# Kernel optimization log

Measured on AMD Instinct MI355X. Metric: run time of the kernel, lower is better.

Reference implementation:

```python
import jax, jax.numpy as jnp
import numpy as np

LN_EPS = 1e-5

def setup_inputs() -> dict:
    key = jax.random.key(0)
    k1, k2, k3 = jax.random.split(key, 3)
    B, Lq, Lk, D = 16, 2048, 2048, 128
    return {
        "query": jax.random.normal(k1, (B, Lq, D), dtype=jnp.float32),
        "key": jax.random.normal(k2, (B, Lk, D), dtype=jnp.float32),
        "value": jax.random.normal(k3, (B, Lk, D), dtype=jnp.float32),
        "attn_mask": jnp.zeros((Lq, Lk), dtype=jnp.float32),
        "gamma": jnp.ones((D,), dtype=jnp.float32),
        "beta": jnp.zeros((D,), dtype=jnp.float32),
    }

def reference(query, key, value, attn_mask, gamma, beta):
    # NOTE: original code does NOT scale by 1/sqrt(d) despite the class name.
    scores = jnp.einsum("bqd,bkd->bqk", query, key)          # [B,Lq,Lk]
    scores = scores + attn_mask[None, :, :]
    probs = jax.nn.softmax(scores, axis=-1)
    out = jnp.einsum("bqk,bkd->bqd", probs, value)            # [B,Lq,D]
    # dropout is identity (eval / rate 0)
    mu = jnp.mean(out, axis=-1, keepdims=True)
    var = jnp.var(out, axis=-1, keepdims=True)
    normed = (out - mu) * jax.lax.rsqrt(var + LN_EPS)
    return normed * gamma + beta
```

## Files before the change

kernel.cpp:

```cpp
#include <hip/hip_runtime.h>
#include <hip/hip_bf16.h>
#include <hip/hip_fp16.h>
#include <math.h>

#define LQ_  2048
#define LK_  2048
#define D_   128
#define B_   16
#define LN_EPS 1e-5f
#define TK_  32
#define NTILE (LK_ / TK_)

#define KH_TILE_US 4096
#define VT_TILE_U  2048
#define KH_BYTES   ((size_t)B_ * NTILE * KH_TILE_US * 2)
#define VT_OFF     KH_BYTES

typedef __attribute__((ext_vector_type(8))) short short8;
typedef __attribute__((ext_vector_type(8))) _Float16 half8;
typedef __attribute__((ext_vector_type(4))) float f32x4;

union FragU { uint4 u4; short8 s8; half8 h8; unsigned int u[4]; };

__device__ __forceinline__ unsigned int pk_bf16(float a, float b) {
  __hip_bfloat162 h = __float22bfloat162_rn(make_float2(a, b));
  unsigned int u;
  __builtin_memcpy(&u, &h, 4);
  return u;
}
__device__ __forceinline__ unsigned short bf16_bits(float x) {
  return (unsigned short)(pk_bf16(x, 0.f) & 0xffffu);
}
__device__ __forceinline__ unsigned int pk_f16(float a, float b) {
  __half2 h = __floats2half2_rn(a, b);
  unsigned int u;
  __builtin_memcpy(&u, &h, 4);
  return u;
}
__device__ __forceinline__ float f16_lo(unsigned int u) {
  unsigned short s = (unsigned short)(u & 0xffffu);
  __half h; __builtin_memcpy(&h, &s, 2); return __half2float(h);
}
__device__ __forceinline__ float f16_hi(unsigned int u) {
  unsigned short s = (unsigned short)(u >> 16);
  __half h; __builtin_memcpy(&h, &s, 2); return __half2float(h);
}

__device__ __forceinline__ int idxK(int row, int d) {
  return row * 128 + ((((d >> 3) ^ row) & 15) << 3) + (d & 7);
}
__device__ __forceinline__ int idxVt(int d, int kp) {
  return d * 16 + ((((kp >> 2) + (d >> 1)) & 3) << 2) + (kp & 3);
}
__device__ __forceinline__ int idxPs(int row, int col) {
  return row * 32 + ((((col >> 3) ^ (row >> 2)) & 3) << 3) + (col & 7);
}

__device__ __forceinline__ void barrier_stage() {
  asm volatile("s_waitcnt vmcnt(8) lgkmcnt(0)\n\ts_barrier" ::: "memory");
}
__device__ __forceinline__ void fence_lds_local() {
  asm volatile("s_waitcnt lgkmcnt(0)" ::: "memory");
}

__device__ __forceinline__ void gld_lds16(const void* g, void* l) {
  __builtin_amdgcn_global_load_lds((const __attribute__((address_space(1))) void*)g,
                                   (__attribute__((address_space(3))) void*)l, 16, 0, 0);
}

__global__ __launch_bounds__(256) void conv_kv(
    const float* __restrict__ kg, const float* __restrict__ vg,
    unsigned short* __restrict__ khg, unsigned int* __restrict__ vtg)
{
  __shared__ float Vlt[128 * 33];
  const int tid = threadIdx.x;
  const int blk = blockIdx.x;
  const int b = blk >> 6;
  const int t = blk & 63;

  const float* ks = kg + ((size_t)b * LK_ + t * 32) * D_;
  const float* vs = vg + ((size_t)b * LK_ + t * 32) * D_;
  unsigned short* kh = khg + (size_t)blk * KH_TILE_US;
  unsigned int*   vt = vtg + (size_t)blk * VT_TILE_U;

#pragma unroll
  for (int it = 0; it < 2; it++) {
    const int item = tid + it * 256;
    const int row = item >> 4;
    const int c8  = item & 15;
    const float* p = ks + row * D_ + c8 * 8;
    float4 x = *(const float4*)(p);
    float4 y = *(const float4*)(p + 4);
    FragU H;
    H.u[0] = pk_f16(x.x, x.y); H.u[1] = pk_f16(x.z, x.w);
    H.u[2] = pk_f16(y.x, y.y); H.u[3] = pk_f16(y.z, y.w);
    *(uint4*)&kh[idxK(row, c8 * 8)] = H.u4;
  }

#pragma unroll
  for (int i = 0; i < 4; i++) {
    const int item = tid + i * 256;
    const int r = item >> 5, c4 = item & 31;
    float4 x = *(const float4*)&vs[r * D_ + c4 * 4];
    Vlt[(c4 * 4 + 0) * 33 + r] = x.x;
    Vlt[(c4 * 4 + 1) * 33 + r] = x.y;
    Vlt[(c4 * 4 + 2) * 33 + r] = x.z;
    Vlt[(c4 * 4 + 3) * 33 + r] = x.w;
  }
  __syncthreads();

#pragma unroll
  for (int i = 0; i < 8; i++) {
    const int o = tid + i * 256;
    const int d = o >> 4, s = o & 15;
    const int gq = s >> 2, c = s & 3;
    const int kp = (((gq - (d >> 1)) & 3) << 2) | c;
    vt[o] = pk_bf16(Vlt[d * 33 + 2 * kp], Vlt[d * 33 + 2 * kp + 1]);
  }
}

__device__ __forceinline__ void stage_tile(int w, int lane,
    const unsigned short* khT, const unsigned int* vtT,
    int tile, unsigned short* khs, unsigned int* vts)
{
  const char* gkh = (const char*)(khT + (size_t)tile * KH_TILE_US);
  const char* gvt = (const char*)(vtT + (size_t)tile * VT_TILE_U);
#pragma unroll
  for (int c = 0; c < 2; c++) {
    const int off = (w + 4 * c) << 10;
    gld_lds16(gkh + off + lane * 16, (char*)khs + off);
    gld_lds16(gvt + off + lane * 16, (char*)vts + off);
  }
}

__global__ __launch_bounds__(256, 2) void attn_ln_mfma(
    const float* __restrict__ qg, const float* __restrict__ maskg,
    const float* __restrict__ gammag, const float* __restrict__ betag,
    const unsigned short* __restrict__ khg, const unsigned int* __restrict__ vtg,
    float* __restrict__ outg)
{
  __shared__ unsigned short KhS[2][32 * 128];
  __shared__ unsigned int   VtW[2][128 * 16];
  __shared__ unsigned short PsS[64 * 32];

  const int tid  = threadIdx.x;
  const int w    = tid >> 6;
  const int lane = tid & 63;
  const int quad = lane >> 4;
  const int lr   = lane & 15;

  const int id   = blockIdx.x;
  const int xcd  = id & 7;
  const int slot = id >> 3;
  const int b    = xcd * 2 + (slot >> 5);
  const int q0   = (slot & 31) * 64;

  const unsigned short* khT = khg + (size_t)b * NTILE * KH_TILE_US;
  const unsigned int*   vtT = vtg + (size_t)b * NTILE * VT_TILE_U;

  const float* mbase = maskg + (size_t)(q0 + w * 16 + quad * 4) * LK_ + lr;

  stage_tile(w, lane, khT, vtT, 0, &KhS[0][0], &VtW[0][0]);
  float mA[2][4], mB[2][4];
#pragma unroll
  for (int ct = 0; ct < 2; ct++)
#pragma unroll
    for (int reg = 0; reg < 4; reg++)
      mA[ct][reg] = mbase[(size_t)reg * LK_ + ct * 16];

  half8 qh[4], ql[4];
  {
    const float* qrow = qg + ((size_t)b * LQ_ + q0 + w * 16 + lr) * D_ + quad * 8;
#pragma unroll
    for (int c = 0; c < 4; c++) {
      float4 x = *(const float4*)(qrow + c * 32);
      float4 y = *(const float4*)(qrow + c * 32 + 4);
      FragU H, L;
      H.u[0] = pk_f16(x.x, x.y); H.u[1] = pk_f16(x.z, x.w);
      H.u[2] = pk_f16(y.x, y.y); H.u[3] = pk_f16(y.z, y.w);
      L.u[0] = pk_f16(x.x - f16_lo(H.u[0]), x.y - f16_hi(H.u[0]));
      L.u[1] = pk_f16(x.z - f16_lo(H.u[1]), x.w - f16_hi(H.u[1]));
      L.u[2] = pk_f16(y.x - f16_lo(H.u[2]), y.y - f16_hi(H.u[2]));
      L.u[3] = pk_f16(y.z - f16_lo(H.u[3]), y.w - f16_hi(H.u[3]));
      qh[c] = H.h8; ql[c] = L.h8;
    }
  }

  float l_part[4] = {0.f, 0.f, 0.f, 0.f};
  f32x4 o[8];
  const f32x4 zf = {0.f, 0.f, 0.f, 0.f};
#pragma unroll
  for (int n = 0; n < 8; n++) o[n] = zf;

  auto body = [&](int kt, int cur, float (&mu)[2][4], float (&mp)[2][4])
      __attribute__((always_inline)) -> void {
    const unsigned short* khc = &KhS[cur][0];
    const unsigned int*   vtc = &VtW[cur][0];

    barrier_stage();

    if (kt + 1 < NTILE) {
      stage_tile(w, lane, khT, vtT, kt + 1, &KhS[cur ^ 1][0], &VtW[cur ^ 1][0]);
#pragma unroll
      for (int ct = 0; ct < 2; ct++)
#pragma unroll
        for (int reg = 0; reg < 4; reg++)
          mp[ct][reg] = mbase[(size_t)reg * LK_ + (kt + 1) * TK_ + ct * 16];
    }

    f32x4 sH[2], sL[2];
    sH[0] = zf; sH[1] = zf; sL[0] = zf; sL[1] = zf;
#pragma unroll
    for (int c = 0; c < 4; c++) {
#pragma unroll
      for (int ct = 0; ct < 2; ct++) {
        FragU kh;
        kh.u4 = *(const uint4*)&khc[idxK(ct * 16 + lr, c * 32 + quad * 8)];
        sH[ct] = __builtin_amdgcn_mfma_f32_16x16x32_f16(qh[c], kh.h8, sH[ct], 0, 0, 0);
        sL[ct] = __builtin_amdgcn_mfma_f32_16x16x32_f16(ql[c], kh.h8, sL[ct], 0, 0, 0);
      }
    }

    FragU Bv[8];
#pragma unroll
    for (int nb = 0; nb < 8; nb++)
      Bv[nb].u4 = *(const uint4*)&vtc[idxVt(nb * 16 + lr, quad * 4)];

#pragma unroll
    for (int ct = 0; ct < 2; ct++)
#pragma unroll
      for (int reg = 0; reg < 4; reg++) {
        float s = sH[ct][reg] + sL[ct][reg];
        float p = __expf(s + mu[ct][reg]);
        l_part[reg] += p;
        PsS[idxPs(w * 16 + quad * 4 + reg, ct * 16 + lr)] = bf16_bits(p);
      }

    fence_lds_local();

    FragU A;
    A.u4 = *(const uint4*)&PsS[idxPs(w * 16 + lr, quad * 8)];
#pragma unroll
    for (int nb = 0; nb < 8; nb++)
      o[nb] = __builtin_amdgcn_mfma_f32_16x16x32_bf16(A.s8, Bv[nb].s8, o[nb], 0, 0, 0);
  };

  for (int kt = 0; kt < NTILE; kt += 2) {
    body(kt,     0, mA, mB);
    body(kt + 1, 1, mB, mA);
  }

  float inv_l[4];
#pragma unroll
  for (int reg = 0; reg < 4; reg++) {
    float l = l_part[reg];
#pragma unroll
    for (int m = 1; m <= 8; m <<= 1) l += __shfl_xor(l, m, 64);
    inv_l[reg] = 1.f / l;
  }

  float gam[8], bet[8];
#pragma unroll
  for (int nb = 0; nb < 8; nb++) {
    gam[nb] = gammag[nb * 16 + lr];
    bet[nb] = betag[nb * 16 + lr];
  }

#pragma unroll
  for (int reg = 0; reg < 4; reg++) {
    float s1 = 0.f, s2 = 0.f;
#pragma unroll
    for (int nb = 0; nb < 8; nb++) {
      float v = o[nb][reg] * inv_l[reg];
      o[nb][reg] = v;
      s1 += v; s2 += v * v;
    }
#pragma unroll
    for (int m = 1; m <= 8; m <<= 1) {
      s1 += __shfl_xor(s1, m, 64);
      s2 += __shfl_xor(s2, m, 64);
    }
    const float mean = s1 * (1.f / 128.f);
    const float var  = s2 * (1.f / 128.f) - mean * mean;
    const float rstd = rsqrtf(var + LN_EPS);

    float* op = outg + ((size_t)b * LQ_ + q0 + w * 16 + quad * 4 + reg) * D_ + lr;
#pragma unroll
    for (int nb = 0; nb < 8; nb++)
      op[nb * 16] = (o[nb][reg] - mean) * rstd * gam[nb] + bet[nb];
  }
}

extern "C" void kernel_launch(void* const* d_in, const int* in_sizes, int n_in,
                              void* d_out, int out_size, void* d_ws, size_t ws_size,
                              hipStream_t stream) {
  const float* q     = (const float*)d_in[0];
  const float* k     = (const float*)d_in[1];
  const float* v     = (const float*)d_in[2];
  const float* mask  = (const float*)d_in[3];
  const float* gamma = (const float*)d_in[4];
  const float* beta  = (const float*)d_in[5];
  float* out = (float*)d_out;

  unsigned short* khg = (unsigned short*)d_ws;
  unsigned int*   vtg = (unsigned int*)((char*)d_ws + VT_OFF);

  conv_kv<<<dim3(B_ * NTILE), dim3(256), 0, stream>>>(k, v, khg, vtg);
  attn_ln_mfma<<<dim3(512), dim3(256), 0, stream>>>(q, mask, gamma, beta,
                                                    khg, vtg, out);
}
```

Measured before the change: 174.4 us.

## Split key tiles across two wave groups per block with LDS reduction

Doubles the block to 512 threads and has two groups of four waves each process alternating key tiles for the same 64 query rows, with separate double-buffered LDS staging per group. After the loop, the second group writes its partial output accumulators and row sums to LDS and the first group adds them before normalization and LayerNorm. This aims to raise waves per CU and halve the serial key loop per block, at the cost of more LDS, an extra reduction phase and idle waves in the epilogue.

Result: slower. 414.4 us (+137.6%).

```diff
diff --git a/kernel.cpp b/kernel.cpp
--- a/kernel.cpp
+++ b/kernel.cpp
@@ -10,11 +10,14 @@
 #define LN_EPS 1e-5f
 #define TK_  32
 #define NTILE (LK_ / TK_)
+#define NBODY (NTILE / 2)
 
 #define KH_TILE_US 4096
 #define VT_TILE_U  2048
 #define KH_BYTES   ((size_t)B_ * NTILE * KH_TILE_US * 2)
 #define VT_OFF     KH_BYTES
+
+#define LDS_TOTAL 73728
 
 typedef __attribute__((ext_vector_type(8))) short short8;
 typedef __attribute__((ext_vector_type(8))) _Float16 half8;
@@ -58,6 +61,9 @@
 
 __device__ __forceinline__ void barrier_stage() {
   asm volatile("s_waitcnt vmcnt(8) lgkmcnt(0)\n\ts_barrier" ::: "memory");
+}
+__device__ __forceinline__ void barrier_lds() {
+  asm volatile("s_waitcnt lgkmcnt(0)\n\ts_barrier" ::: "memory");
 }
 __device__ __forceinline__ void fence_lds_local() {
   asm volatile("s_waitcnt lgkmcnt(0)" ::: "memory");
@@ -119,32 +125,32 @@
   }
 }
 
-__device__ __forceinline__ void stage_tile(int w, int lane,
+__device__ __forceinline__ void stage_tile(int wr, int lane,
     const unsigned short* khT, const unsigned int* vtT,
-    int tile, unsigned short* khs, unsigned int* vts)
+    int tile, char* khs, char* vts)
 {
   const char* gkh = (const char*)(khT + (size_t)tile * KH_TILE_US);
   const char* gvt = (const char*)(vtT + (size_t)tile * VT_TILE_U);
 #pragma unroll
   for (int c = 0; c < 2; c++) {
-    const int off = (w + 4 * c) << 10;
-    gld_lds16(gkh + off + lane * 16, (char*)khs + off);
-    gld_lds16(gvt + off + lane * 16, (char*)vts + off);
-  }
-}
-
-__global__ __launch_bounds__(256, 2) void attn_ln_mfma(
+    const int off = (wr + 4 * c) << 10;
+    gld_lds16(gkh + off + lane * 16, khs + off);
+    gld_lds16(gvt + off + lane * 16, vts + off);
+  }
+}
+
+__global__ __launch_bounds__(512, 4) void attn_ln_mfma(
     const float* __restrict__ qg, const float* __restrict__ maskg,
     const float* __restrict__ gammag, const float* __restrict__ betag,
     const unsigned short* __restrict__ khg, const unsigned int* __restrict__ vtg,
     float* __restrict__ outg)
 {
-  __shared__ unsigned short KhS[2][32 * 128];
-  __shared__ unsigned int   VtW[2][128 * 16];
-  __shared__ unsigned short PsS[64 * 32];
+  __shared__ __align__(16) char LB[LDS_TOTAL];
 
   const int tid  = threadIdx.x;
   const int w    = tid >> 6;
+  const int ts   = w >> 2;
+  const int wr   = w & 3;
   const int lane = tid & 63;
   const int quad = lane >> 4;
   const int lr   = lane & 15;
@@ -158,19 +164,25 @@
   const unsigned short* khT = khg + (size_t)b * NTILE * KH_TILE_US;
   const unsigned int*   vtT = vtg + (size_t)b * NTILE * VT_TILE_U;
 
-  const float* mbase = maskg + (size_t)(q0 + w * 16 + quad * 4) * LK_ + lr;
-
-  stage_tile(w, lane, khT, vtT, 0, &KhS[0][0], &VtW[0][0]);
+  char* khB0 = LB + (ts * 2 + 0) * 8192;
+  char* khB1 = LB + (ts * 2 + 1) * 8192;
+  char* vtB0 = LB + 32768 + (ts * 2 + 0) * 8192;
+  char* vtB1 = LB + 32768 + (ts * 2 + 1) * 8192;
+  unsigned short* Ps = (unsigned short*)(LB + 65536);
+
+  const float* mbase = maskg + (size_t)(q0 + wr * 16 + quad * 4) * LK_ + lr;
+
+  stage_tile(wr, lane, khT, vtT, ts, khB0, vtB0);
   float mA[2][4], mB[2][4];
 #pragma unroll
   for (int ct = 0; ct < 2; ct++)
 #pragma unroll
     for (int reg = 0; reg < 4; reg++)
-      mA[ct][reg] = mbase[(size_t)reg * LK_ + ct * 16];
+      mA[ct][reg] = mbase[(size_t)reg * LK_ + ts * TK_ + ct * 16];
 
   half8 qh[4], ql[4];
   {
-    const float* qrow = qg + ((size_t)b * LQ_ + q0 + w * 16 + lr) * D_ + quad * 8;
+    const float* qrow = qg + ((size_t)b * LQ_ + q0 + wr * 16 + lr) * D_ + quad * 8;
 #pragma unroll
     for (int c = 0; c < 4; c++) {
       float4 x = *(const float4*)(qrow + c * 32);
@@ -192,20 +204,21 @@
 #pragma unroll
   for (int n = 0; n < 8; n++) o[n] = zf;
 
-  auto body = [&](int kt, int cur, float (&mu)[2][4], float (&mp)[2][4])
+  auto body = [&](int i, int cur, float (&mu)[2][4], float (&mp)[2][4])
       __attribute__((always_inline)) -> void {
-    const unsigned short* khc = &KhS[cur][0];
-    const unsigned int*   vtc = &VtW[cur][0];
+    const unsigned short* khc = (const unsigned short*)(cur ? khB1 : khB0);
+    const unsigned int*   vtc = (const unsigned int*)(cur ? vtB1 : vtB0);
+    const int mt = 2 * i + ts;
 
     barrier_stage();
 
-    if (kt + 1 < NTILE) {
-      stage_tile(w, lane, khT, vtT, kt + 1, &KhS[cur ^ 1][0], &VtW[cur ^ 1][0]);
+    if (i + 1 < NBODY) {
+      stage_tile(wr, lane, khT, vtT, mt + 2, cur ? khB0 : khB1, cur ? vtB0 : vtB1);
 #pragma unroll
       for (int ct = 0; ct < 2; ct++)
 #pragma unroll
         for (int reg = 0; reg < 4; reg++)
-          mp[ct][reg] = mbase[(size_t)reg * LK_ + (kt + 1) * TK_ + ct * 16];
+          mp[ct][reg] = mbase[(size_t)reg * LK_ + (mt + 2) * TK_ + ct * 16];
     }
 
     f32x4 sH[2], sL[2];
@@ -233,61 +246,87 @@
         float s = sH[ct][reg] + sL[ct][reg];
         float p = __expf(s + mu[ct][reg]);
         l_part[reg] += p;
-        PsS[idxPs(w * 16 + quad * 4 + reg, ct * 16 + lr)] = bf16_bits(p);
+        Ps[idxPs(w * 16 + quad * 4 + reg, ct * 16 + lr)] = bf16_bits(p);
       }
 
     fence_lds_local();
 
     FragU A;
-    A.u4 = *(const uint4*)&PsS[idxPs(w * 16 + lr, quad * 8)];
+    A.u4 = *(const uint4*)&Ps[idxPs(w * 16 + lr, quad * 8)];
 #pragma unroll
     for (int nb = 0; nb < 8; nb++)
       o[nb] = __builtin_amdgcn_mfma_f32_16x16x32_bf16(A.s8, Bv[nb].s8, o[nb], 0, 0, 0);
   };
 
-  for (int kt = 0; kt < NTILE; kt += 2) {
-    body(kt,     0, mA, mB);
-    body(kt + 1, 1, mB, mA);
-  }
-
-  float inv_l[4];
-#pragma unroll
-  for (int reg = 0; reg < 4; reg++) {
-    float l = l_part[reg];
-#pragma unroll
-    for (int m = 1; m <= 8; m <<= 1) l += __shfl_xor(l, m, 64);
-    inv_l[reg] = 1.f / l;
-  }
-
-  float gam[8], bet[8];
-#pragma unroll
-  for (int nb = 0; nb < 8; nb++) {
-    gam[nb] = gammag[nb * 16 + lr];
-    bet[nb] = betag[nb * 16 + lr];
-  }
-
-#pragma unroll
-  for (int reg = 0; reg < 4; reg++) {
-    float s1 = 0.f, s2 = 0.f;
+  for (int i = 0; i < NBODY; i += 2) {
+    body(i,     0, mA, mB);
+    body(i + 1, 1, mB, mA);
+  }
+
+  float* exch = (float*)LB + (size_t)wr * 64 * 37 + (size_t)lane * 37;
+
+  barrier_lds();
+  if (ts == 1) {
+#pragma unroll
+    for (int nb = 0; nb < 8; nb++)
+#pragma unroll
+      for (int reg = 0; reg < 4; reg++)
+        exch[nb * 4 + reg] = o[nb][reg];
+#pragma unroll
+    for (int reg = 0; reg < 4; reg++)
+      exch[32 + reg] = l_part[reg];
+  }
+  barrier_lds();
+
+  if (ts == 0) {
+#pragma unroll
+    for (int nb = 0; nb < 8; nb++)
+#pragma unroll
+      for (int reg = 0; reg < 4; reg++)
+        o[nb][reg] += exch[nb * 4 + reg];
+#pragma unroll
+    for (int reg = 0; reg < 4; reg++)
+      l_part[reg] += exch[32 + reg];
+
+    float inv_l[4];
+#pragma unroll
+    for (int reg = 0; reg < 4; reg++) {
+      float l = l_part[reg];
+#pragma unroll
+      for (int m = 1; m <= 8; m <<= 1) l += __shfl_xor(l, m, 64);
+      inv_l[reg] = 1.f / l;
+    }
+
+    float gam[8], bet[8];
 #pragma unroll
     for (int nb = 0; nb < 8; nb++) {
-      float v = o[nb][reg] * inv_l[reg];
-      o[nb][reg] = v;
-      s1 += v; s2 += v * v;
-    }
-#pragma unroll
-    for (int m = 1; m <= 8; m <<= 1) {
-      s1 += __shfl_xor(s1, m, 64);
-      s2 += __shfl_xor(s2, m, 64);
-    }
-    const float mean = s1 * (1.f / 128.f);
-    const float var  = s2 * (1.f / 128.f) - mean * mean;
-    const float rstd = rsqrtf(var + LN_EPS);
-
-    float* op = outg + ((size_t)b * LQ_ + q0 + w * 16 + quad * 4 + reg) * D_ + lr;
-#pragma unroll
-    for (int nb = 0; nb < 8; nb++)
-      op[nb * 16] = (o[nb][reg] - mean) * rstd * gam[nb] + bet[nb];
+      gam[nb] = gammag[nb * 16 + lr];
+      bet[nb] = betag[nb * 16 + lr];
+    }
+
+#pragma unroll
+    for (int reg = 0; reg < 4; reg++) {
+      float s1 = 0.f, s2 = 0.f;
+#pragma unroll
+      for (int nb = 0; nb < 8; nb++) {
+        float v = o[nb][reg] * inv_l[reg];
+        o[nb][reg] = v;
+        s1 += v; s2 += v * v;
+      }
+#pragma unroll
+      for (int m = 1; m <= 8; m <<= 1) {
+        s1 += __shfl_xor(s1, m, 64);
+        s2 += __shfl_xor(s2, m, 64);
+      }
+      const float mean = s1 * (1.f / 128.f);
+      const float var  = s2 * (1.f / 128.f) - mean * mean;
+      const float rstd = rsqrtf(var + LN_EPS);
+
+      float* op = outg + ((size_t)b * LQ_ + q0 + wr * 16 + quad * 4 + reg) * D_ + lr;
+#pragma unroll
+      for (int nb = 0; nb < 8; nb++)
+        op[nb * 16] = (o[nb][reg] - mean) * rstd * gam[nb] + bet[nb];
+    }
   }
 }
 
@@ -306,6 +345,6 @@
   unsigned int*   vtg = (unsigned int*)((char*)d_ws + VT_OFF);
 
   conv_kv<<<dim3(B_ * NTILE), dim3(256), 0, stream>>>(k, v, khg, vtg);
-  attn_ln_mfma<<<dim3(512), dim3(256), 0, stream>>>(q, mask, gamma, beta,
+  attn_ln_mfma<<<dim3(512), dim3(512), 0, stream>>>(q, mask, gamma, beta,
                                                     khg, vtg, out);
 }
```

## Swap QK MFMA operands to keep P in registers and skip the LDS round-trip

Applied to the files above, without the earlier changes.

Computes S transposed by swapping the MFMA A and B operands, so each lane holds probabilities in the layout the PV MFMA needs as its A fragment. P is then packed into bf16 in registers, which removes the PsS shared buffer, its stores and reload, and the LDS fence. V^T is repacked in the prep kernel so its k ordering matches the new P fragment order. The mask is now loaded as float4 per row, and the row sum is reduced across quads and then redistributed with shuffles. The waitcnt threshold is also changed to vmcnt(2) to match the fewer outstanding loads.

New measurement: 182.0 us. 1.04x slower.

```diff
diff --git a/kernel.cpp b/kernel.cpp
--- a/kernel.cpp
+++ b/kernel.cpp
@@ -28,9 +28,6 @@
   __builtin_memcpy(&u, &h, 4);
   return u;
 }
-__device__ __forceinline__ unsigned short bf16_bits(float x) {
-  return (unsigned short)(pk_bf16(x, 0.f) & 0xffffu);
-}
 __device__ __forceinline__ unsigned int pk_f16(float a, float b) {
   __half2 h = __floats2half2_rn(a, b);
   unsigned int u;
@@ -49,18 +46,12 @@
 __device__ __forceinline__ int idxK(int row, int d) {
   return row * 128 + ((((d >> 3) ^ row) & 15) << 3) + (d & 7);
 }
-__device__ __forceinline__ int idxVt(int d, int kp) {
-  return d * 16 + ((((kp >> 2) + (d >> 1)) & 3) << 2) + (kp & 3);
-}
-__device__ __forceinline__ int idxPs(int row, int col) {
-  return row * 32 + ((((col >> 3) ^ (row >> 2)) & 3) << 3) + (col & 7);
+__device__ __forceinline__ int idxVt(int d, int slot) {
+  return d * 16 + ((((slot >> 2) + (d >> 1)) & 3) << 2) + (slot & 3);
 }
 
 __device__ __forceinline__ void barrier_stage() {
-  asm volatile("s_waitcnt vmcnt(8) lgkmcnt(0)\n\ts_barrier" ::: "memory");
-}
-__device__ __forceinline__ void fence_lds_local() {
-  asm volatile("s_waitcnt lgkmcnt(0)" ::: "memory");
+  asm volatile("s_waitcnt vmcnt(2) lgkmcnt(0)\n\ts_barrier" ::: "memory");
 }
 
 __device__ __forceinline__ void gld_lds16(const void* g, void* l) {
@@ -112,24 +103,25 @@
 #pragma unroll
   for (int i = 0; i < 8; i++) {
     const int o = tid + i * 256;
-    const int d = o >> 4, s = o & 15;
-    const int gq = s >> 2, c = s & 3;
-    const int kp = (((gq - (d >> 1)) & 3) << 2) | c;
+    const int d = o >> 4, sp = o & 15;
+    const int gl = ((sp >> 2) - (d >> 1)) & 3;
+    const int c  = sp & 3;
+    const int kp = 2 * gl + ((c >> 1) << 3) + (c & 1);
     vt[o] = pk_bf16(Vlt[d * 33 + 2 * kp], Vlt[d * 33 + 2 * kp + 1]);
   }
 }
 
 __device__ __forceinline__ void stage_tile(int w, int lane,
     const unsigned short* khT, const unsigned int* vtT,
-    int tile, unsigned short* khs, unsigned int* vts)
+    int tile, char* khs, char* vts)
 {
   const char* gkh = (const char*)(khT + (size_t)tile * KH_TILE_US);
   const char* gvt = (const char*)(vtT + (size_t)tile * VT_TILE_U);
 #pragma unroll
   for (int c = 0; c < 2; c++) {
     const int off = (w + 4 * c) << 10;
-    gld_lds16(gkh + off + lane * 16, (char*)khs + off);
-    gld_lds16(gvt + off + lane * 16, (char*)vts + off);
+    gld_lds16(gkh + off + lane * 16, khs + off);
+    gld_lds16(gvt + off + lane * 16, vts + off);
   }
 }
 
@@ -141,7 +133,6 @@
 {
   __shared__ unsigned short KhS[2][32 * 128];
   __shared__ unsigned int   VtW[2][128 * 16];
-  __shared__ unsigned short PsS[64 * 32];
 
   const int tid  = threadIdx.x;
   const int w    = tid >> 6;
@@ -158,15 +149,12 @@
   const unsigned short* khT = khg + (size_t)b * NTILE * KH_TILE_US;
   const unsigned int*   vtT = vtg + (size_t)b * NTILE * VT_TILE_U;
 
-  const float* mbase = maskg + (size_t)(q0 + w * 16 + quad * 4) * LK_ + lr;
-
-  stage_tile(w, lane, khT, vtT, 0, &KhS[0][0], &VtW[0][0]);
-  float mA[2][4], mB[2][4];
-#pragma unroll
-  for (int ct = 0; ct < 2; ct++)
-#pragma unroll
-    for (int reg = 0; reg < 4; reg++)
-      mA[ct][reg] = mbase[(size_t)reg * LK_ + ct * 16];
+  const float* mrow = maskg + (size_t)(q0 + w * 16 + lr) * LK_ + quad * 4;
+
+  stage_tile(w, lane, khT, vtT, 0, (char*)&KhS[0][0], (char*)&VtW[0][0]);
+  float4 mA[2], mB[2];
+  mA[0] = *(const float4*)(mrow);
+  mA[1] = *(const float4*)(mrow + 16);
 
   half8 qh[4], ql[4];
   {
@@ -186,13 +174,13 @@
     }
   }
 
-  float l_part[4] = {0.f, 0.f, 0.f, 0.f};
+  float l_part = 0.f;
   f32x4 o[8];
   const f32x4 zf = {0.f, 0.f, 0.f, 0.f};
 #pragma unroll
   for (int n = 0; n < 8; n++) o[n] = zf;
 
-  auto body = [&](int kt, int cur, float (&mu)[2][4], float (&mp)[2][4])
+  auto body = [&](int kt, int cur, float4 (&mu)[2], float4 (&mp)[2])
       __attribute__((always_inline)) -> void {
     const unsigned short* khc = &KhS[cur][0];
     const unsigned int*   vtc = &VtW[cur][0];
@@ -200,12 +188,10 @@
     barrier_stage();
 
     if (kt + 1 < NTILE) {
-      stage_tile(w, lane, khT, vtT, kt + 1, &KhS[cur ^ 1][0], &VtW[cur ^ 1][0]);
-#pragma unroll
-      for (int ct = 0; ct < 2; ct++)
-#pragma unroll
-        for (int reg = 0; reg < 4; reg++)
-          mp[ct][reg] = mbase[(size_t)reg * LK_ + (kt + 1) * TK_ + ct * 16];
+      stage_tile(w, lane, khT, vtT, kt + 1,
+                 (char*)&KhS[cur ^ 1][0], (char*)&VtW[cur ^ 1][0]);
+      mp[0] = *(const float4*)(mrow + (kt + 1) * TK_);
+      mp[1] = *(const float4*)(mrow + (kt + 1) * TK_ + 16);
     }
 
     f32x4 sH[2], sL[2];
@@ -216,8 +202,8 @@
       for (int ct = 0; ct < 2; ct++) {
         FragU kh;
         kh.u4 = *(const uint4*)&khc[idxK(ct * 16 + lr, c * 32 + quad * 8)];
-        sH[ct] = __builtin_amdgcn_mfma_f32_16x16x32_f16(qh[c], kh.h8, sH[ct], 0, 0, 0);
-        sL[ct] = __builtin_amdgcn_mfma_f32_16x16x32_f16(ql[c], kh.h8, sL[ct], 0, 0, 0);
+        sH[ct] = __builtin_amdgcn_mfma_f32_16x16x32_f16(kh.h8, qh[c], sH[ct], 0, 0, 0);
+        sL[ct] = __builtin_amdgcn_mfma_f32_16x16x32_f16(kh.h8, ql[c], sL[ct], 0, 0, 0);
       }
     }
 
@@ -226,20 +212,24 @@
     for (int nb = 0; nb < 8; nb++)
       Bv[nb].u4 = *(const uint4*)&vtc[idxVt(nb * 16 + lr, quad * 4)];
 
-#pragma unroll
-    for (int ct = 0; ct < 2; ct++)
+    float pv[2][4];
+#pragma unroll
+    for (int ct = 0; ct < 2; ct++) {
+      const float* mf = (const float*)&mu[ct];
 #pragma unroll
       for (int reg = 0; reg < 4; reg++) {
-        float s = sH[ct][reg] + sL[ct][reg];
-        float p = __expf(s + mu[ct][reg]);
-        l_part[reg] += p;
-        PsS[idxPs(w * 16 + quad * 4 + reg, ct * 16 + lr)] = bf16_bits(p);
+        float p = __expf(sH[ct][reg] + sL[ct][reg] + mf[reg]);
+        l_part += p;
+        pv[ct][reg] = p;
       }
-
-    fence_lds_local();
+    }
 
     FragU A;
-    A.u4 = *(const uint4*)&PsS[idxPs(w * 16 + lr, quad * 8)];
+    A.u[0] = pk_bf16(pv[0][0], pv[0][1]);
+    A.u[1] = pk_bf16(pv[0][2], pv[0][3]);
+    A.u[2] = pk_bf16(pv[1][0], pv[1][1]);
+    A.u[3] = pk_bf16(pv[1][2], pv[1][3]);
+
 #pragma unroll
     for (int nb = 0; nb < 8; nb++)
       o[nb] = __builtin_amdgcn_mfma_f32_16x16x32_bf16(A.s8, Bv[nb].s8, o[nb], 0, 0, 0);
@@ -250,14 +240,15 @@
     body(kt + 1, 1, mB, mA);
   }
 
+  float lt = l_part;
+  lt += __shfl_xor(lt, 16, 64);
+  lt += __shfl_xor(lt, 32, 64);
+  const float invl = 1.f / lt;
+
   float inv_l[4];
 #pragma unroll
-  for (int reg = 0; reg < 4; reg++) {
-    float l = l_part[reg];
-#pragma unroll
-    for (int m = 1; m <= 8; m <<= 1) l += __shfl_xor(l, m, 64);
-    inv_l[reg] = 1.f / l;
-  }
+  for (int reg = 0; reg < 4; reg++)
+    inv_l[reg] = __shfl(invl, quad * 20 + reg, 64);
 
   float gam[8], bet[8];
 #pragma unroll
```
